# Optimization experiments

Measured on AMD Instinct MI355X. Metric: run time of the kernel, lower is better.

Reference implementation:

```python
import jax, jax.numpy as jnp
import numpy as np

N_NODES = 50000
N_EDGES = 800000
IN_CH = 128
HID = 32
HEADS = 4
OUT_CH = 16
NEG_SLOPE = 0.2  # PyG GATConv default LeakyReLU slope


def setup_inputs() -> dict:
    key = jax.random.key(0)
    ks = jax.random.split(key, 12)
    x = jax.random.normal(ks[0], (N_NODES, IN_CH), dtype=jnp.float32)
    edge_index = jax.random.randint(ks[1], (2, N_EDGES), 0, N_NODES, dtype=jnp.int32)
    edge_attr = jax.random.uniform(ks[2], (N_EDGES,), dtype=jnp.float32)
    s = 0.1
    W1 = jax.random.normal(ks[3], (IN_CH, HEADS * HID), dtype=jnp.float32) * s
    a_src1 = jax.random.normal(ks[4], (HEADS, HID), dtype=jnp.float32) * s
    a_dst1 = jax.random.normal(ks[5], (HEADS, HID), dtype=jnp.float32) * s
    b1 = jnp.zeros((HEADS * HID,), dtype=jnp.float32)
    W2 = jax.random.normal(ks[6], (HEADS * HID, OUT_CH), dtype=jnp.float32) * s
    a_src2 = jax.random.normal(ks[7], (1, OUT_CH), dtype=jnp.float32) * s
    a_dst2 = jax.random.normal(ks[8], (1, OUT_CH), dtype=jnp.float32) * s
    b2 = jnp.zeros((OUT_CH,), dtype=jnp.float32)
    return {"x": x, "edge_index": edge_index, "edge_attr": edge_attr,
            "W1": W1, "a_src1": a_src1, "a_dst1": a_dst1, "b1": b1,
            "W2": W2, "a_src2": a_src2, "a_dst2": a_dst2, "b2": b2}


def gat_conv(x, src, dst, num_nodes, W, a_src, a_dst, bias, concat):
    H, C = a_src.shape
    h = (x @ W).reshape(-1, H, C)              # [N,H,C]
    al_src = jnp.sum(h * a_src, axis=-1)       # [N,H]
    al_dst = jnp.sum(h * a_dst, axis=-1)       # [N,H]
    e = jax.nn.leaky_relu(al_src[src] + al_dst[dst], NEG_SLOPE)  # [E,H]
    # segment softmax over incoming edges of each destination node
    m = jax.ops.segment_max(e, dst, num_segments=num_nodes)
    ex = jnp.exp(e - m[dst])
    denom = jax.ops.segment_sum(ex, dst, num_segments=num_nodes)
    alpha = ex / (denom[dst] + 1e-16)          # [E,H]
    out = jax.ops.segment_sum(h[src] * alpha[..., None], dst, num_segments=num_nodes)  # [N,H,C]
    out = out.reshape(num_nodes, H * C) if concat else out.mean(axis=1)
    return out + bias


def reference(x, edge_index, edge_attr, W1, a_src1, a_dst1, b1, W2, a_src2, a_dst2, b2):
    # edge_attr is ignored by GATConv when edge_dim is None (PyG default)
    N = x.shape[0]
    loop = jnp.arange(N, dtype=edge_index.dtype)  # PyG add_self_loops=True
    src = jnp.concatenate([edge_index[0], loop])
    dst = jnp.concatenate([edge_index[1], loop])
    h = jax.nn.elu(gat_conv(x, src, dst, N, W1, a_src1, a_dst1, b1, True))
    out = gat_conv(h, src, dst, N, W2, a_src2, a_dst2, b2, False)
    return jax.nn.log_softmax(out, axis=1)
```

## Files before the change

### kernel.cpp

```cpp
#include <hip/hip_runtime.h>

#define N_NODESC 50000
#define E0C      800000
#define E_TOTC   850000
#define IN_CHC   128
#define HCC      128
#define HEADSC   4
#define OUT_CHC  16
#define NEG_SLOPE 0.2f
#define G1M      64
#define NBUCK    196
#define BNODES   256
#define SBLK     128
#define CHUNK    6656

typedef __attribute__((ext_vector_type(8))) short bf16x8;
typedef __attribute__((ext_vector_type(4))) float f32x4;

__device__ __forceinline__ float lrelu(float v){ return v > 0.f ? v : NEG_SLOPE * v; }

__device__ __forceinline__ unsigned int f2bf(float f){
  unsigned int b = __float_as_uint(f);
  return (b + 0x7fffu + ((b >> 16) & 1u)) >> 16;
}
__device__ __forceinline__ float bf2f(unsigned int lo16){
  return __uint_as_float(lo16 << 16);
}

__global__ void __launch_bounds__(256) k_gemm1(const float* __restrict__ x, const float* __restrict__ W1,
        const float* __restrict__ a_s, const float* __restrict__ a_d,
        unsigned int* __restrict__ h1b, float* __restrict__ al_s, float* __restrict__ al_d)
{
  __shared__ __align__(16) unsigned short Wt[IN_CHC*HCC];
  __shared__ __align__(16) unsigned short xt[G1M*IN_CHC];
  int tid = threadIdx.x, lane = tid & 63, wave = tid >> 6;
  int row0 = blockIdx.x * G1M;

  for (int n0 = 0; n0 < 128; n0 += 64){
    int n = n0 + wave*16 + (lane & 15);
    for (int kc = 0; kc < 128; kc += 32){
      int k = kc + (lane >> 4)*8;
      unsigned int u[4];
      #pragma unroll
      for (int j = 0; j < 8; j += 2){
        float a = W1[(size_t)(k+j)*HCC + n];
        float b = W1[(size_t)(k+j+1)*HCC + n];
        u[j>>1] = f2bf(a) | (f2bf(b) << 16);
      }
      int idx = (n*128 + k) ^ ((n & 7) << 3);
      *(uint4*)&Wt[idx] = make_uint4(u[0],u[1],u[2],u[3]);
    }
  }
  {
    int r  = tid >> 2;
    int kc = (tid & 3) * 32;
    int rr = row0 + r; if (rr > N_NODESC-1) rr = N_NODESC-1;
    const float* xp = &x[(size_t)rr*IN_CHC + kc];
    #pragma unroll
    for (int j = 0; j < 32; j += 8){
      unsigned int u0 = f2bf(xp[j+0]) | (f2bf(xp[j+1]) << 16);
      unsigned int u1 = f2bf(xp[j+2]) | (f2bf(xp[j+3]) << 16);
      unsigned int u2 = f2bf(xp[j+4]) | (f2bf(xp[j+5]) << 16);
      unsigned int u3 = f2bf(xp[j+6]) | (f2bf(xp[j+7]) << 16);
      int idx = (r*128 + kc + j) ^ ((r & 7) << 3);
      *(uint4*)&xt[idx] = make_uint4(u0,u1,u2,u3);
    }
  }
  __syncthreads();

  int rw = wave * 16;
  f32x4 acc[8];
  #pragma unroll
  for (int t = 0; t < 8; t++) acc[t] = (f32x4){0.f,0.f,0.f,0.f};
  #pragma unroll
  for (int kk = 0; kk < 128; kk += 32){
    int m  = rw + (lane & 15);
    int ks = kk + (lane >> 4)*8;
    bf16x8 afrag = *(bf16x8*)&xt[(m*128 + ks) ^ ((m & 7) << 3)];
    #pragma unroll
    for (int t = 0; t < 8; t++){
      int n = t*16 + (lane & 15);
      bf16x8 bfrag = *(bf16x8*)&Wt[(n*128 + ks) ^ ((n & 7) << 3)];
      acc[t] = __builtin_amdgcn_mfma_f32_16x16x32_bf16(afrag, bfrag, acc[t], 0, 0, 0);
    }
  }

  float asv[8], adv[8];
  #pragma unroll
  for (int t = 0; t < 8; t++){
    asv[t] = a_s[t*16 + (lane & 15)];
    adv[t] = a_d[t*16 + (lane & 15)];
  }
  #pragma unroll
  for (int r = 0; r < 4; r++){
    int row = row0 + rw + (lane >> 4)*4 + r;
    bool ok = (row < N_NODESC);
    #pragma unroll
    for (int t = 0; t < 8; t++){
      float v = acc[t][r];
      float o = __shfl_xor(v, 1, 64);
      int c = t*16 + (lane & 15);
      if (ok && ((c & 1) == 0))
        h1b[(size_t)row*64 + (c >> 1)] = f2bf(v) | (f2bf(o) << 16);
    }
    #pragma unroll
    for (int h = 0; h < 4; h++){
      float ps = acc[2*h][r]*asv[2*h] + acc[2*h+1][r]*asv[2*h+1];
      float pd = acc[2*h][r]*adv[2*h] + acc[2*h+1][r]*adv[2*h+1];
      #pragma unroll
      for (int m = 1; m < 16; m <<= 1){ ps += __shfl_xor(ps, m, 64); pd += __shfl_xor(pd, m, 64); }
      if (ok && (lane & 15) == 0){
        al_s[row*HEADSC + h] = ps;
        al_d[row*HEADSC + h] = pd;
      }
    }
  }
}

__global__ void __launch_bounds__(256) k_binA(const int* __restrict__ ei, int* __restrict__ bh){
  __shared__ int h[NBUCK];
  int tid = threadIdx.x, b = blockIdx.x;
  for (int i = tid; i < NBUCK; i += 256) h[i] = 0;
  __syncthreads();
  int e0 = b*CHUNK, e1 = e0 + CHUNK; if (e1 > E_TOTC) e1 = E_TOTC;
  for (int e = e0 + tid; e < e1; e += 256){
    int d = (e < E0C) ? ei[E0C + e] : (e - E0C);
    atomicAdd(&h[d >> 8], 1);
  }
  __syncthreads();
  for (int i = tid; i < NBUCK; i += 256) bh[b*NBUCK + i] = h[i];
}

__global__ void __launch_bounds__(256) k_binscan(int* __restrict__ bh, int* __restrict__ bstart){
  __shared__ int buf[256];
  int tid = threadIdx.x;
  int tot = 0;
  if (tid < NBUCK)
    for (int b = 0; b < SBLK; b++) tot += bh[b*NBUCK + tid];
  buf[tid] = (tid < NBUCK) ? tot : 0;
  __syncthreads();
  #pragma unroll
  for (int off = 1; off < 256; off <<= 1){
    int t = (tid >= off) ? buf[tid - off] : 0;
    __syncthreads();
    buf[tid] += t; __syncthreads();
  }
  int excl = buf[tid] - ((tid < NBUCK) ? tot : 0);
  if (tid < NBUCK) bstart[tid] = excl;
  if (tid == 0) bstart[NBUCK] = E_TOTC;
  __syncthreads();
  if (tid < NBUCK){
    int run = excl;
    for (int b = 0; b < SBLK; b++){
      int t = bh[b*NBUCK + tid];
      bh[b*NBUCK + tid] = run;
      run += t;
    }
  }
}

__global__ void __launch_bounds__(256) k_binB(const int* __restrict__ ei, const int* __restrict__ bh,
                                              unsigned int* __restrict__ binbuf){
  __shared__ int h[NBUCK];
  int tid = threadIdx.x, b = blockIdx.x;
  for (int i = tid; i < NBUCK; i += 256) h[i] = bh[b*NBUCK + i];
  __syncthreads();
  int e0 = b*CHUNK, e1 = e0 + CHUNK; if (e1 > E_TOTC) e1 = E_TOTC;
  for (int e = e0 + tid; e < e1; e += 256){
    int s, d;
    if (e < E0C){ d = ei[E0C + e]; s = ei[e]; }
    else { s = e - E0C; d = s; }
    int pos = atomicAdd(&h[d >> 8], 1);
    binbuf[pos] = ((unsigned int)d << 16) | (unsigned int)s;
  }
}

__global__ void __launch_bounds__(256) k_binC(const unsigned int* __restrict__ binbuf,
                                              const int* __restrict__ bstart,
                                              int* __restrict__ rp, int* __restrict__ srcs){
  __shared__ int lcnt[BNODES];
  __shared__ int buf[BNODES];
  __shared__ int pfx[BNODES];
  int tid = threadIdx.x, k = blockIdx.x;
  int lo = k * BNODES;
  int b0 = bstart[k], b1 = bstart[k+1];
  lcnt[tid] = 0;
  __syncthreads();
  for (int i = b0 + tid; i < b1; i += 256){
    int d = binbuf[i] >> 16;
    atomicAdd(&lcnt[d - lo], 1);
  }
  __syncthreads();
  int v = lcnt[tid];
  buf[tid] = v;
  __syncthreads();
  #pragma unroll
  for (int off = 1; off < 256; off <<= 1){
    int t = (tid >= off) ? buf[tid - off] : 0;
    __syncthreads();
    buf[tid] += t; __syncthreads();
  }
  int excl = buf[tid] - v;
  pfx[tid] = excl;
  int node = lo + tid;
  if (node < N_NODESC) rp[node] = b0 + excl;
  if (k == 0 && tid == 0) rp[N_NODESC] = E_TOTC;
  lcnt[tid] = 0;
  __syncthreads();
  for (int i = b0 + tid; i < b1; i += 256){
    unsigned int u = binbuf[i];
    int d = u >> 16;
    int r = atomicAdd(&lcnt[d - lo], 1);
    srcs[b0 + pfx[d - lo] + r] = (int)(u & 0xffffu);
  }
}

__global__ void __launch_bounds__(256) k_node1(const unsigned int* __restrict__ h1b,
        const float* __restrict__ al_s, const float* __restrict__ al_d,
        const int* __restrict__ rp, const int* __restrict__ srcs,
        const float* __restrict__ b1, float* __restrict__ hout)
{
  int wave = threadIdx.x >> 6, lane = threadIdx.x & 63;
  int n = blockIdx.x*4 + wave;
  if (n >= N_NODESC) return;
  int beg = rp[n], end = rp[n+1];
  int h = lane >> 4;
  float adh = al_d[n*4 + h];
  float dsum = 0.f, acc0 = 0.f, acc1 = 0.f;
  #pragma unroll 4
  for (int p = beg; p < end; p++){
    int s = srcs[p];
    float a = __expf(lrelu(al_s[s*4 + h] + adh));
    unsigned int u = h1b[(size_t)s*64 + lane];
    dsum += a;
    acc0 = fmaf(a, bf2f(u & 0xffffu), acc0);
    acc1 = fmaf(a, bf2f(u >> 16), acc1);
  }
  float inv = 1.f / (dsum + 1e-16f);
  int c0 = lane*2;
  float o0 = acc0*inv + b1[c0], o1 = acc1*inv + b1[c0+1];
  o0 = o0 > 0.f ? o0 : __expf(o0) - 1.f;
  o1 = o1 > 0.f ? o1 : __expf(o1) - 1.f;
  *(float2*)&hout[(size_t)n*HCC + c0] = make_float2(o0, o1);
}

__global__ void __launch_bounds__(256) k_gemm2(const float* __restrict__ hin, const float* __restrict__ W2,
        const float* __restrict__ a_s, const float* __restrict__ a_d,
        unsigned int* __restrict__ h2b, float* __restrict__ al_s, float* __restrict__ al_d)
{
  __shared__ __align__(16) float Wl[IN_CHC*OUT_CHC];
  __shared__ __align__(16) float xr[4][4][IN_CHC];
  int tid = threadIdx.x;
  for (int i = tid*4; i < IN_CHC*OUT_CHC; i += 256*4)
    *(float4*)&Wl[i] = *(const float4*)&W2[i];
  __syncthreads();
  int wave = tid >> 6, lane = tid & 63;
  int r = lane >> 4, c = lane & 15;
  int row0 = blockIdx.x*16 + wave*4;
  for (int rr = 0; rr < 4; rr++){
    float2 v = *(const float2*)&hin[(size_t)(row0+rr)*IN_CHC + lane*2];
    *(float2*)&xr[wave][rr][lane*2] = v;
  }
  float acc = 0.f;
  #pragma unroll 8
  for (int k = 0; k < IN_CHC; k++)
    acc = fmaf(xr[wave][r][k], Wl[k*OUT_CHC + c], acc);
  int row = row0 + r;
  float other = __shfl_xor(acc, 1, 64);
  if ((c & 1) == 0)
    h2b[(size_t)row*8 + (c >> 1)] = f2bf(acc) | (f2bf(other) << 16);
  float ps = acc * a_s[c];
  float pd = acc * a_d[c];
  #pragma unroll
  for (int m = 1; m < 16; m <<= 1){ ps += __shfl_xor(ps, m, 64); pd += __shfl_xor(pd, m, 64); }
  if (c == 0){ al_s[row] = ps; al_d[row] = pd; }
}

__global__ void __launch_bounds__(256) k_node2(const unsigned int* __restrict__ h2b,
        const float* __restrict__ al_s, const float* __restrict__ al_d,
        const int* __restrict__ rp, const int* __restrict__ srcs,
        const float* __restrict__ b2, float* __restrict__ out)
{
  int wave = threadIdx.x >> 6, lane = threadIdx.x & 63;
  int n = blockIdx.x*4 + wave;
  if (n >= N_NODESC) return;
  int beg = rp[n], end = rp[n+1];
  float ad = al_d[n];
  int c = lane & 15, jg = lane >> 4;
  unsigned int hi = (c & 1);
  int widx = c >> 1;
  float dsum = 0.f, acc = 0.f;
  #pragma unroll 4
  for (int p = beg + jg; p < end; p += 4){
    int s = srcs[p];
    float a = __expf(lrelu(al_s[s] + ad));
    unsigned int u = h2b[(size_t)s*8 + widx];
    float hv = __uint_as_float(hi ? (u & 0xFFFF0000u) : (u << 16));
    dsum += a;
    acc = fmaf(a, hv, acc);
  }
  dsum += __shfl_xor(dsum, 16, 64);
  dsum += __shfl_xor(dsum, 32, 64);
  acc += __shfl_xor(acc, 16, 64);
  acc += __shfl_xor(acc, 32, 64);
  float inv = 1.f / (dsum + 1e-16f);
  float v = acc*inv + b2[c];
  float mm = v;
  #pragma unroll
  for (int o = 1; o < 16; o <<= 1) mm = fmaxf(mm, __shfl_xor(mm, o, 64));
  float se = __expf(v - mm);
  #pragma unroll
  for (int o = 1; o < 16; o <<= 1) se += __shfl_xor(se, o, 64);
  if (jg == 0) out[n*OUT_CHC + c] = v - mm - __logf(se);
}

extern "C" void kernel_launch(void* const* d_in, const int* in_sizes, int n_in,
                              void* d_out, int out_size, void* d_ws, size_t ws_size,
                              hipStream_t stream)
{
  const float* x   = (const float*)d_in[0];
  const int*   ei  = (const int*)d_in[1];
  const float* W1  = (const float*)d_in[3];
  const float* as1 = (const float*)d_in[4];
  const float* ad1 = (const float*)d_in[5];
  const float* b1  = (const float*)d_in[6];
  const float* W2  = (const float*)d_in[7];
  const float* as2 = (const float*)d_in[8];
  const float* ad2 = (const float*)d_in[9];
  const float* b2  = (const float*)d_in[10];
  float* out = (float*)d_out;

  char* ws = (char*)d_ws;
  size_t off = 0;
  auto alloc = [&](size_t bytes)->void*{
    void* p = ws + off;
    off = (off + bytes + 255) & ~(size_t)255;
    return p;
  };
  unsigned int* h1b = (unsigned int*)alloc((size_t)N_NODESC*64*4);
  float* hout  = (float*)alloc((size_t)N_NODESC*HCC*4);
  float* al_s1 = (float*)alloc((size_t)N_NODESC*HEADSC*4);
  float* al_d1 = (float*)alloc((size_t)N_NODESC*HEADSC*4);
  unsigned int* h2b = (unsigned int*)alloc((size_t)N_NODESC*8*4);
  float* al_s2 = (float*)alloc((size_t)N_NODESC*4);
  float* al_d2 = (float*)alloc((size_t)N_NODESC*4);
  int* rp      = (int*)alloc((size_t)(N_NODESC+1)*4);
  int* srcs    = (int*)alloc((size_t)E_TOTC*4);
  int* bh      = (int*)alloc((size_t)SBLK*NBUCK*4);
  int* bstart  = (int*)alloc((size_t)(NBUCK+1)*4);
  unsigned int* binbuf = (unsigned int*)alloc((size_t)E_TOTC*4);

  k_gemm1<<<(N_NODESC+G1M-1)/G1M, 256, 0, stream>>>(x, W1, as1, ad1, h1b, al_s1, al_d1);
  k_binA<<<SBLK, 256, 0, stream>>>(ei, bh);
  k_binscan<<<1, 256, 0, stream>>>(bh, bstart);
  k_binB<<<SBLK, 256, 0, stream>>>(ei, bh, binbuf);
  k_binC<<<NBUCK, 256, 0, stream>>>(binbuf, bstart, rp, srcs);
  k_node1<<<(N_NODESC+3)/4, 256, 0, stream>>>(h1b, al_s1, al_d1, rp, srcs, b1, hout);
  k_gemm2<<<N_NODESC/16, 256, 0, stream>>>(hout, W2, as2, ad2, h2b, al_s2, al_d2);
  k_node2<<<(N_NODESC+3)/4, 256, 0, stream>>>(h2b, al_s2, al_d2, rp, srcs, b2, out);
}
```

Baseline: 150.2 us.

## Fuse bin histogram into gemm1 launch, store srcs as u16 and hidden as bf16

Adds the edge-bucket histogram blocks to the gemm1 grid so both run in one launch and the separate k_binA kernel goes away. Source indices are now stored as 16-bit values, halving CSR index traffic in both aggregation kernels. The layer-1 output is written as packed bf16 instead of fp32, halving the write in node1 and the read in gemm2. This adds rounding error in the second layer's input.

```diff
diff --git a/kernel.cpp b/kernel.cpp
--- a/kernel.cpp
+++ b/kernel.cpp
@@ -9,6 +9,7 @@
 #define OUT_CHC  16
 #define NEG_SLOPE 0.2f
 #define G1M      64
+#define NG1      ((N_NODESC + G1M - 1)/G1M)
 #define NBUCK    196
 #define BNODES   256
 #define SBLK     128
@@ -27,15 +28,31 @@
   return __uint_as_float(lo16 << 16);
 }
 
-__global__ void __launch_bounds__(256) k_gemm1(const float* __restrict__ x, const float* __restrict__ W1,
+__global__ void __launch_bounds__(256) k_gemm1A(const float* __restrict__ x, const float* __restrict__ W1,
         const float* __restrict__ a_s, const float* __restrict__ a_d,
-        unsigned int* __restrict__ h1b, float* __restrict__ al_s, float* __restrict__ al_d)
+        unsigned int* __restrict__ h1b, float* __restrict__ al_s, float* __restrict__ al_d,
+        const int* __restrict__ ei, int* __restrict__ bh)
 {
   __shared__ __align__(16) unsigned short Wt[IN_CHC*HCC];
   __shared__ __align__(16) unsigned short xt[G1M*IN_CHC];
+  __shared__ int hh[NBUCK];
   int tid = threadIdx.x, lane = tid & 63, wave = tid >> 6;
+
+  if (blockIdx.x >= NG1){
+    int b = blockIdx.x - NG1;
+    for (int i = tid; i < NBUCK; i += 256) hh[i] = 0;
+    __syncthreads();
+    int e0 = b*CHUNK, e1 = e0 + CHUNK; if (e1 > E_TOTC) e1 = E_TOTC;
+    for (int e = e0 + tid; e < e1; e += 256){
+      int d = (e < E0C) ? ei[E0C + e] : (e - E0C);
+      atomicAdd(&hh[d >> 8], 1);
+    }
+    __syncthreads();
+    for (int i = tid; i < NBUCK; i += 256) bh[b*NBUCK + i] = hh[i];
+    return;
+  }
+
   int row0 = blockIdx.x * G1M;
-
   for (int n0 = 0; n0 < 128; n0 += 64){
     int n = n0 + wave*16 + (lane & 15);
     for (int kc = 0; kc < 128; kc += 32){
@@ -117,20 +134,6 @@
   }
 }
 
-__global__ void __launch_bounds__(256) k_binA(const int* __restrict__ ei, int* __restrict__ bh){
-  __shared__ int h[NBUCK];
-  int tid = threadIdx.x, b = blockIdx.x;
-  for (int i = tid; i < NBUCK; i += 256) h[i] = 0;
-  __syncthreads();
-  int e0 = b*CHUNK, e1 = e0 + CHUNK; if (e1 > E_TOTC) e1 = E_TOTC;
-  for (int e = e0 + tid; e < e1; e += 256){
-    int d = (e < E0C) ? ei[E0C + e] : (e - E0C);
-    atomicAdd(&h[d >> 8], 1);
-  }
-  __syncthreads();
-  for (int i = tid; i < NBUCK; i += 256) bh[b*NBUCK + i] = h[i];
-}
-
 __global__ void __launch_bounds__(256) k_binscan(int* __restrict__ bh, int* __restrict__ bstart){
   __shared__ int buf[256];
   int tid = threadIdx.x;
@@ -177,7 +180,7 @@
 
 __global__ void __launch_bounds__(256) k_binC(const unsigned int* __restrict__ binbuf,
                                               const int* __restrict__ bstart,
-                                              int* __restrict__ rp, int* __restrict__ srcs){
+                                              int* __restrict__ rp, unsigned short* __restrict__ srcs){
   __shared__ int lcnt[BNODES];
   __shared__ int buf[BNODES];
   __shared__ int pfx[BNODES];
@@ -211,14 +214,14 @@
     unsigned int u = binbuf[i];
     int d = u >> 16;
     int r = atomicAdd(&lcnt[d - lo], 1);
-    srcs[b0 + pfx[d - lo] + r] = (int)(u & 0xffffu);
+    srcs[b0 + pfx[d - lo] + r] = (unsigned short)(u & 0xffffu);
   }
 }
 
 __global__ void __launch_bounds__(256) k_node1(const unsigned int* __restrict__ h1b,
         const float* __restrict__ al_s, const float* __restrict__ al_d,
-        const int* __restrict__ rp, const int* __restrict__ srcs,
-        const float* __restrict__ b1, float* __restrict__ hout)
+        const int* __restrict__ rp, const unsigned short* __restrict__ srcs,
+        const float* __restrict__ b1, unsigned int* __restrict__ houtb)
 {
   int wave = threadIdx.x >> 6, lane = threadIdx.x & 63;
   int n = blockIdx.x*4 + wave;
@@ -241,10 +244,10 @@
   float o0 = acc0*inv + b1[c0], o1 = acc1*inv + b1[c0+1];
   o0 = o0 > 0.f ? o0 : __expf(o0) - 1.f;
   o1 = o1 > 0.f ? o1 : __expf(o1) - 1.f;
-  *(float2*)&hout[(size_t)n*HCC + c0] = make_float2(o0, o1);
-}
-
-__global__ void __launch_bounds__(256) k_gemm2(const float* __restrict__ hin, const float* __restrict__ W2,
+  houtb[(size_t)n*64 + lane] = f2bf(o0) | (f2bf(o1) << 16);
+}
+
+__global__ void __launch_bounds__(256) k_gemm2(const unsigned int* __restrict__ hinb, const float* __restrict__ W2,
         const float* __restrict__ a_s, const float* __restrict__ a_d,
         unsigned int* __restrict__ h2b, float* __restrict__ al_s, float* __restrict__ al_d)
 {
@@ -258,8 +261,9 @@
   int r = lane >> 4, c = lane & 15;
   int row0 = blockIdx.x*16 + wave*4;
   for (int rr = 0; rr < 4; rr++){
-    float2 v = *(const float2*)&hin[(size_t)(row0+rr)*IN_CHC + lane*2];
-    *(float2*)&xr[wave][rr][lane*2] = v;
+    unsigned int u = hinb[(size_t)(row0+rr)*64 + lane];
+    xr[wave][rr][lane*2]   = bf2f(u & 0xffffu);
+    xr[wave][rr][lane*2+1] = bf2f(u >> 16);
   }
   float acc = 0.f;
   #pragma unroll 8
@@ -278,7 +282,7 @@
 
 __global__ void __launch_bounds__(256) k_node2(const unsigned int* __restrict__ h2b,
         const float* __restrict__ al_s, const float* __restrict__ al_d,
-        const int* __restrict__ rp, const int* __restrict__ srcs,
+        const int* __restrict__ rp, const unsigned short* __restrict__ srcs,
         const float* __restrict__ b2, float* __restrict__ out)
 {
   int wave = threadIdx.x >> 6, lane = threadIdx.x & 63;
@@ -338,24 +342,23 @@
     return p;
   };
   unsigned int* h1b = (unsigned int*)alloc((size_t)N_NODESC*64*4);
-  float* hout  = (float*)alloc((size_t)N_NODESC*HCC*4);
+  unsigned int* houtb = (unsigned int*)alloc((size_t)N_NODESC*64*4);
   float* al_s1 = (float*)alloc((size_t)N_NODESC*HEADSC*4);
   float* al_d1 = (float*)alloc((size_t)N_NODESC*HEADSC*4);
   unsigned int* h2b = (unsigned int*)alloc((size_t)N_NODESC*8*4);
   float* al_s2 = (float*)alloc((size_t)N_NODESC*4);
   float* al_d2 = (float*)alloc((size_t)N_NODESC*4);
   int* rp      = (int*)alloc((size_t)(N_NODESC+1)*4);
-  int* srcs    = (int*)alloc((size_t)E_TOTC*4);
+  unsigned short* srcs = (unsigned short*)alloc((size_t)E_TOTC*2);
   int* bh      = (int*)alloc((size_t)SBLK*NBUCK*4);
   int* bstart  = (int*)alloc((size_t)(NBUCK+1)*4);
   unsigned int* binbuf = (unsigned int*)alloc((size_t)E_TOTC*4);
 
-  k_gemm1<<<(N_NODESC+G1M-1)/G1M, 256, 0, stream>>>(x, W1, as1, ad1, h1b, al_s1, al_d1);
-  k_binA<<<SBLK, 256, 0, stream>>>(ei, bh);
+  k_gemm1A<<<NG1 + SBLK, 256, 0, stream>>>(x, W1, as1, ad1, h1b, al_s1, al_d1, ei, bh);
   k_binscan<<<1, 256, 0, stream>>>(bh, bstart);
   k_binB<<<SBLK, 256, 0, stream>>>(ei, bh, binbuf);
   k_binC<<<NBUCK, 256, 0, stream>>>(binbuf, bstart, rp, srcs);
-  k_node1<<<(N_NODESC+3)/4, 256, 0, stream>>>(h1b, al_s1, al_d1, rp, srcs, b1, hout);
-  k_gemm2<<<N_NODESC/16, 256, 0, stream>>>(hout, W2, as2, ad2, h2b, al_s2, al_d2);
-  k_node2<<<(N_NODESC+3)/4, 256, 0, stream>>>(h2b, al_s2, al_d2, rp, srcs, b2, out);
-}
+  k_node1<<<N_NODESC/4, 256, 0, stream>>>(h1b, al_s1, al_d1, rp, srcs, b1, houtb);
+  k_gemm2<<<N_NODESC/16, 256, 0, stream>>>(houtb, W2, as2, ad2, h2b, al_s2, al_d2);
+  k_node2<<<N_NODESC/4, 256, 0, stream>>>(h2b, al_s2, al_d2, rp, srcs, b2, out);
+}
```

Result: faster. 140.0 us, median of 2 (-6.7%).
